# Kernel optimization log

Hardware: AMD Instinct MI355X
Metric: run time of the kernel (lower is better)

Reference implementation:

```python
import jax, jax.numpy as jnp
import numpy as np

B = 32
T_CAP = 63            # max_caption_length - 1
VOCAB = 32000
IMG_DIM = 20480
EMB = 512
LSTM_DIM = 500


def setup_inputs() -> dict:
    key = jax.random.key(0)
    ks = jax.random.split(key, 10)
    s = 0.02
    return {
        "input_image": jax.random.normal(ks[0], (B, IMG_DIM), dtype=jnp.float32),
        "input_caption": jax.random.randint(ks[1], (B, T_CAP), 0, VOCAB, dtype=jnp.int32),
        # image_embedding Dense
        "W_img": jax.random.normal(ks[2], (IMG_DIM, EMB), dtype=jnp.float32) * s,
        "b_img": jnp.zeros((EMB,), dtype=jnp.float32),
        # caption_embedding table
        "emb": jax.random.normal(ks[3], (VOCAB, EMB), dtype=jnp.float32) * s,
        # LSTM kernels (keras gate order: i, f, c, o)
        "W_lstm": jax.random.normal(ks[4], (EMB, 4 * LSTM_DIM), dtype=jnp.float32) * s,
        "U_lstm": jax.random.normal(ks[5], (LSTM_DIM, 4 * LSTM_DIM), dtype=jnp.float32) * s,
        "b_lstm": jnp.concatenate([jnp.zeros((LSTM_DIM,)), jnp.ones((LSTM_DIM,)),
                                    jnp.zeros((2 * LSTM_DIM,))]).astype(jnp.float32),  # unit forget bias
        # output Dense + softmax
        "W_out": jax.random.normal(ks[6], (LSTM_DIM, VOCAB), dtype=jnp.float32) * s,
        "b_out": jnp.zeros((VOCAB,), dtype=jnp.float32),
    }


def _lstm_scan(x, W, U, b):
    # x: [B, T, EMB] -> outputs [B, T, LSTM_DIM]
    Bx = x.shape[0]
    # precompute input projections for all timesteps (one big GEMM)
    xz = jnp.einsum('btd,dg->btg', x, W) + b  # [B, T, 4H]
    xz = jnp.swapaxes(xz, 0, 1)               # [T, B, 4H]
    h0 = jnp.zeros((Bx, LSTM_DIM), dtype=x.dtype)
    c0 = jnp.zeros((Bx, LSTM_DIM), dtype=x.dtype)

    def step(carry, z_t):
        h, c = carry
        z = z_t + h @ U                        # [B, 4H]
        i, f, g, o = jnp.split(z, 4, axis=-1)  # keras gate order i,f,c,o
        i = jax.nn.sigmoid(i)
        f = jax.nn.sigmoid(f)
        g = jnp.tanh(g)
        o = jax.nn.sigmoid(o)
        c_new = f * c + i * g
        h_new = o * jnp.tanh(c_new)
        return (h_new, c_new), h_new

    _, hs = jax.lax.scan(step, (h0, c0), xz)   # hs: [T, B, H]
    return jnp.swapaxes(hs, 0, 1)


def reference(input_image, input_caption, W_img, b_img, emb, W_lstm, U_lstm, b_lstm, W_out, b_out):
    # image embedding -> one leading timestep
    x_image = (input_image @ W_img + b_img)[:, None, :]      # [B, 1, EMB]
    x_caption = emb[input_caption]                            # [B, T-1, EMB]
    x = jnp.concatenate([x_image, x_caption], axis=1)         # [B, T, EMB]
    h = _lstm_scan(x, W_lstm, U_lstm, b_lstm)                 # [B, T, H]
    logits = jnp.einsum('bth,hv->btv', h, W_out) + b_out      # [B, T, VOCAB]
    return jax.nn.softmax(logits, axis=-1)
```

## Files before the change

### kernel.cpp

```cpp
#include <hip/hip_runtime.h>

typedef float f32x4 __attribute__((ext_vector_type(4)));
typedef short s16x8 __attribute__((ext_vector_type(8)));
typedef unsigned int u32;
typedef unsigned long long u64;

#define B_    32
#define T_    64
#define TCAP_ 63
#define V_    32000
#define IMGD_ 20480
#define E_    512
#define H_    500
#define KP_   512

#define OFF_XZ     0ul
#define OFF_XB     16384000ul
#define OFF_WLT    18481152ul
#define OFF_HPAD   20578304ul
#define OFF_HS     20643840ul
#define OFF_UPREP  22740992ul
#define OFF_WT     24838144ul
#define OFF_RS     57606144ul


__device__ __forceinline__ short bf16rn(float f) {
  u32 u = __float_as_uint(f);
  u += 0x7fff + ((u >> 16) & 1);
  return (short)(u >> 16);
}
__device__ __forceinline__ float sigf(float x) {
  return 1.0f / (1.0f + __expf(-x));
}
__device__ __forceinline__ void gload_lds16(const void* g, void* l) {
  __builtin_amdgcn_global_load_lds((const __attribute__((address_space(1))) void*)g,
                                   (__attribute__((address_space(3))) void*)l, 16, 0, 0);
}

#define SG_XB   504
#define SG_X32  520
#define SG_RS   522
#define SG_FL   523
#define SG_UP   4619
#define SG_WT   12619
#define SG_WLT  13131
__global__ __launch_bounds__(256) void k_prep(const float* __restrict__ bimg,
                                              const float* __restrict__ emb,
                                              const int* __restrict__ cap,
                                              const float* __restrict__ U,
                                              const float* __restrict__ Wo,
                                              const float* __restrict__ Wl,
                                              short* __restrict__ xb,
                                              float* __restrict__ x32,
                                              float* __restrict__ rowsum,
                                              u32* __restrict__ flags,
                                              short* __restrict__ up,
                                              short* __restrict__ wt,
                                              short* __restrict__ wlt) {
  __shared__ float s[32][65];
  int bid = blockIdx.x, tid = threadIdx.x;
  if (bid < SG_XB) {
    int u = bid * 256 + tid;
    int r = u >> 6, j8 = u & 63;
    int b = r / 63, tt = r - b * 63;
    int e = cap[b * TCAP_ + tt];
    const float* src = emb + (size_t)e * E_ + j8 * 8;
    f32x4 v0 = *(const f32x4*)src;
    f32x4 v1 = *(const f32x4*)(src + 4);
    s16x8 o;
    o[0]=bf16rn(v0.x); o[1]=bf16rn(v0.y); o[2]=bf16rn(v0.z); o[3]=bf16rn(v0.w);
    o[4]=bf16rn(v1.x); o[5]=bf16rn(v1.y); o[6]=bf16rn(v1.z); o[7]=bf16rn(v1.w);
    *(s16x8*)(xb + (size_t)(b * T_ + tt + 1) * KP_ + j8 * 8) = o;
  } else if (bid < SG_X32) {
    int i = (bid - SG_XB) * 256 + tid;
    int b = i >> 7, j = i & 127;
    *(f32x4*)(x32 + b * E_ + j * 4) = *(const f32x4*)(bimg + j * 4);
  } else if (bid < SG_RS) {
    int i = (bid - SG_X32) * 256 + tid;
    *(f32x4*)(rowsum + i * 4) = (f32x4){0.f, 0.f, 0.f, 0.f};
  } else if (bid < SG_FL) {
    if (tid < 32) flags[tid] = 0u;
  } else if (bid < SG_UP) {
    int idx = (bid - SG_FL) * 256 + tid;
    int k = idx & 511;
    int c = (idx >> 9) & 63;
    int wg = idx >> 15;
    int q = c >> 4, dl = c & 15, dg = wg * 16 + dl;
    float v = 0.f;
    if (dg < H_ && k < H_) v = U[(size_t)k * 2000 + q * H_ + dg];
    up[idx] = bf16rn(v);
  } else if (bid < SG_WT) {
    int r = bid - SG_UP;
    int nt = r % 500, kt = r / 500;
    int n0 = nt * 64, k0 = kt * 32;
    for (int u = tid; u < 2048; u += 256) {
      int kl = u >> 6, nl = u & 63;
      int k = k0 + kl;
      s[kl][nl] = (k < H_) ? Wo[(size_t)k * V_ + n0 + nl] : 0.f;
    }
    __syncthreads();
    for (int u = tid; u < 2048; u += 256) {
      int nl = u >> 5, kl = u & 31;
      wt[(size_t)(n0 + nl) * KP_ + k0 + kl] = bf16rn(s[kl][nl]);
    }
  } else {
    int r = bid - SG_WT;
    int nt = r & 31, kt = r >> 5;
    int n0 = nt * 64, k0 = kt * 32;
    for (int u = tid; u < 2048; u += 256) {
      int kl = u >> 6, nl = u & 63;
      int n = n0 + nl;
      s[kl][nl] = (n < 2000) ? Wl[(size_t)(k0 + kl) * 2000 + n] : 0.f;
    }
    __syncthreads();
    for (int u = tid; u < 2048; u += 256) {
      int nl = u >> 5, kl = u & 31;
      wlt[(size_t)(n0 + nl) * KP_ + k0 + kl] = bf16rn(s[kl][nl]);
    }
  }
}

__global__ __launch_bounds__(256) void k_img(const float* __restrict__ img,
                                             const float* __restrict__ W,
                                             float* __restrict__ x32) {
  __shared__ float simg[32][128];
  int ct = blockIdx.x & 7;
  int ks = blockIdx.x >> 3;
  int tid = threadIdx.x;
  int j = tid & 63, bq = tid >> 6;
  int col = ct * 64 + j;
  float acc[8] = {0.f, 0.f, 0.f, 0.f, 0.f, 0.f, 0.f, 0.f};
  int kbeg = ks * 1280;
  for (int k0 = kbeg; k0 < kbeg + 1280; k0 += 128) {
    __syncthreads();
    for (int u = tid; u < 32 * 32; u += 256) {
      int b = u >> 5, kq = (u & 31) * 4;
      *(f32x4*)&simg[b][kq] = *(const f32x4*)(img + (size_t)b * IMGD_ + k0 + kq);
    }
    __syncthreads();
    for (int k = 0; k < 128; ++k) {
      float w = W[(size_t)(k0 + k) * E_ + col];
#pragma unroll
      for (int r = 0; r < 8; ++r) acc[r] += simg[bq * 8 + r][k] * w;
    }
  }
#pragma unroll
  for (int r = 0; r < 8; ++r)
    atomicAdd(x32 + (bq * 8 + r) * E_ + col, acc[r]);
}

__global__ __launch_bounds__(256) void k_xb(const float* __restrict__ x32,
                                            short* __restrict__ xb) {
  int u = blockIdx.x * 256 + threadIdx.x;
  int b = u >> 6, j8 = u & 63;
  const float* src = x32 + b * E_ + j8 * 8;
  f32x4 v0 = *(const f32x4*)src;
  f32x4 v1 = *(const f32x4*)(src + 4);
  s16x8 o;
  o[0]=bf16rn(v0.x); o[1]=bf16rn(v0.y); o[2]=bf16rn(v0.z); o[3]=bf16rn(v0.w);
  o[4]=bf16rn(v1.x); o[5]=bf16rn(v1.y); o[6]=bf16rn(v1.z); o[7]=bf16rn(v1.w);
  *(s16x8*)(xb + (size_t)(b * T_) * KP_ + j8 * 8) = o;
}

__global__ __launch_bounds__(256) void k_xzm(const short* __restrict__ A,
                                             const short* __restrict__ Bt,
                                             const float* __restrict__ bl,
                                             float* __restrict__ xz) {
  __shared__ short sA[2][128 * 64];
  __shared__ short sB[2][128 * 64];
  int bid = blockIdx.x;
  int mt = bid & 15, nt = bid >> 4;
  int m0 = mt * 128, n0 = nt * 128;
  int tid = threadIdx.x;
  int lane = tid & 63, w = tid >> 6;
  int wr = w >> 1, wc = w & 1;
  int l15 = lane & 15, l4 = lane >> 4;

  f32x4 acc[4][4];
#pragma unroll
  for (int i = 0; i < 4; ++i)
#pragma unroll
    for (int j = 0; j < 4; ++j) acc[i][j] = (f32x4){0.f, 0.f, 0.f, 0.f};

  auto stage = [&](int kc, int buf) {
    const short* ga = A + (size_t)m0 * KP_ + kc * 64;
    const short* gb = Bt + (size_t)n0 * KP_ + kc * 64;
#pragma unroll
    for (int i = 0; i < 4; ++i) {
      int ch = tid + i * 256;
      int rr = ch >> 3, kq = (ch & 7) * 8;
      gload_lds16(ga + (size_t)rr * KP_ + kq, &sA[buf][rr * 64 + kq]);
      gload_lds16(gb + (size_t)rr * KP_ + kq, &sB[buf][rr * 64 + kq]);
    }
  };

  stage(0, 0);
  __syncthreads();
  int buf = 0;
  for (int kc = 0; kc < 8; ++kc) {
    if (kc < 7) stage(kc + 1, buf ^ 1);
#pragma unroll
    for (int k2 = 0; k2 < 2; ++k2) {
      int kloc = k2 * 32 + l4 * 8;
      s16x8 af[4], bfr[4];
#pragma unroll
      for (int fm = 0; fm < 4; ++fm)
        af[fm] = *(const s16x8*)&sA[buf][(wr * 64 + fm * 16 + l15) * 64 + kloc];
#pragma unroll
      for (int fn = 0; fn < 4; ++fn)
        bfr[fn] = *(const s16x8*)&sB[buf][(wc * 64 + fn * 16 + l15) * 64 + kloc];
#pragma unroll
      for (int fm = 0; fm < 4; ++fm)
#pragma unroll
        for (int fn = 0; fn < 4; ++fn)
          acc[fm][fn] = __builtin_amdgcn_mfma_f32_16x16x32_bf16(af[fm], bfr[fn], acc[fm][fn], 0, 0, 0);
    }
    __syncthreads();
    buf ^= 1;
  }

  float bln[4];
#pragma unroll
  for (int fn = 0; fn < 4; ++fn) {
    int n = n0 + wc * 64 + fn * 16 + l15;
    bln[fn] = (n < 2000) ? bl[n] : 0.f;
  }
#pragma unroll
  for (int fm = 0; fm < 4; ++fm) {
#pragma unroll
    for (int reg = 0; reg < 4; ++reg) {
      int m = m0 + wr * 64 + fm * 16 + l4 * 4 + reg;
      int b = m >> 6, t = m & 63;
#pragma unroll
      for (int fn = 0; fn < 4; ++fn) {
        int n = n0 + wc * 64 + fn * 16 + l15;
        if (n < 2000)
          xz[((size_t)t * B_ + b) * 2000 + n] = acc[fm][fn][reg] + bln[fn];
      }
    }
  }
}

__global__ __launch_bounds__(128) void k_scan(const short* __restrict__ up,
                                              const float* __restrict__ xz,
                                              short* hpad,
                                              short* __restrict__ hs,
                                              u32* flags) {
  __shared__ short Ul[64 * 512];
  int wg = blockIdx.x;
  int tid = threadIdx.x;
  int lane = tid & 63, mtile = tid >> 6;
  int dl = lane & 15, g16 = lane >> 4;

  const short* usrc = up + (size_t)wg * 64 * 512;
  for (int u = tid; u < 4096; u += 128) {
    int c = u >> 6, kq = (u & 63) * 8;
    u32 off = ((u32)(c * 512 + kq) * 2) ^ ((u32)(c & 7) << 4);
    *(s16x8*)((char*)Ul + off) = *(const s16x8*)(usrc + c * 512 + kq);
  }
  __syncthreads();

  int dg = wg * 16 + dl;
  bool dvalid = dg < H_;
  float cst[4] = {0.f, 0.f, 0.f, 0.f};
  int brow = mtile * 16 + dl;

  float xzr[4][4];
  auto pf = [&](int t) {
#pragma unroll
    for (int q = 0; q < 4; ++q)
#pragma unroll
      for (int reg = 0; reg < 4; ++reg) {
        int b = mtile * 16 + g16 * 4 + reg;
        xzr[q][reg] = dvalid ? xz[((size_t)t * B_ + b) * 2000 + q * 500 + dg] : 0.f;
      }
  };
  pf(0);

  for (int t = 0; t < 64; ++t) {
    f32x4 acc[4];
#pragma unroll
    for (int q = 0; q < 4; ++q) acc[q] = (f32x4){0.f, 0.f, 0.f, 0.f};

    if (t > 0) {
      const short* hsrc = hpad + (size_t)(t & 1) * (B_ * KP_);
      u64 q0[16], q1[16];
#pragma unroll
      for (int kk = 0; kk < 16; ++kk) {
        const u64* p = (const u64*)(hsrc + brow * KP_ + kk * 32 + g16 * 8);
        q0[kk] = __hip_atomic_load(p,     __ATOMIC_RELAXED, __HIP_MEMORY_SCOPE_AGENT);
        q1[kk] = __hip_atomic_load(p + 1, __ATOMIC_RELAXED, __HIP_MEMORY_SCOPE_AGENT);
      }
#pragma unroll
      for (int kk = 0; kk < 16; ++kk) {
        union { s16x8 v; u64 q[2]; } fr;
        fr.q[0] = q0[kk]; fr.q[1] = q1[kk];
#pragma unroll
        for (int q = 0; q < 4; ++q) {
          int c = q * 16 + dl;
          u32 off = ((u32)(c * 512 + kk * 32 + g16 * 8) * 2) ^ ((u32)(c & 7) << 4);
          s16x8 bfr = *(const s16x8*)((const char*)Ul + off);
          acc[q] = __builtin_amdgcn_mfma_f32_16x16x32_bf16(fr.v, bfr, acc[q], 0, 0, 0);
        }
      }
    }

    short hb4[4];
#pragma unroll
    for (int reg = 0; reg < 4; ++reg) {
      float zi = acc[0][reg] + xzr[0][reg];
      float zf = acc[1][reg] + xzr[1][reg];
      float zc = acc[2][reg] + xzr[2][reg];
      float zo = acc[3][reg] + xzr[3][reg];
      float ig = sigf(zi), fg = sigf(zf), gt = tanhf(zc), og = sigf(zo);
      float cn = fg * cst[reg] + ig * gt;
      cst[reg] = cn;
      float h = og * tanhf(cn);
      if (!dvalid) h = 0.f;
      hb4[reg] = bf16rn(h);
    }

    short* hnext = hpad + (size_t)((t + 1) & 1) * (B_ * KP_);
#pragma unroll
    for (int reg = 0; reg < 4; ++reg) {
      int mine = (int)(u32)(unsigned short)hb4[reg];
      int oth = __shfl_xor(mine, 1);
      if ((dl & 1) == 0) {
        int b = mtile * 16 + g16 * 4 + reg;
        u32 val = ((u32)mine) | ((u32)oth << 16);
        __hip_atomic_store((u32*)hnext + ((b * KP_ + dg) >> 1), val,
                           __ATOMIC_RELAXED, __HIP_MEMORY_SCOPE_AGENT);
      }
    }

    if (t < 63) {
      __syncthreads();
      if (tid == 0)
        __hip_atomic_store(&flags[wg], (u32)(t + 1),
                           __ATOMIC_RELAXED, __HIP_MEMORY_SCOPE_AGENT);
      asm volatile("" ::: "memory");
#pragma unroll
      for (int reg = 0; reg < 4; ++reg) {
        int b = mtile * 16 + g16 * 4 + reg;
        hs[((size_t)b * T_ + t) * KP_ + dg] = hb4[reg];
      }
      pf(t + 1);
      if (tid < 64) {
        u32 target = (u32)(t + 1);
        int slot = tid & 31;
        while (true) {
          u32 v = __hip_atomic_load(&flags[slot], __ATOMIC_RELAXED,
                                    __HIP_MEMORY_SCOPE_AGENT);
          if (__all(v >= target)) break;
          __builtin_amdgcn_s_sleep(1);
        }
      }
      __syncthreads();
    } else {
#pragma unroll
      for (int reg = 0; reg < 4; ++reg) {
        int b = mtile * 16 + g16 * 4 + reg;
        hs[((size_t)b * T_ + t) * KP_ + dg] = hb4[reg];
      }
    }
  }
}

__global__ __launch_bounds__(256) void k_gemm(const short* __restrict__ A,
                                              const short* __restrict__ Bt,
                                              const float* __restrict__ bout,
                                              float* __restrict__ out,
                                              float* __restrict__ rowsum) {
  __shared__ short sA[2][128 * 64];
  __shared__ short sB[2][128 * 64];
  int bid = blockIdx.x;
  int mt = bid & 15, nt = bid >> 4;
  int m0 = mt * 128, n0 = nt * 128;
  int tid = threadIdx.x;
  int lane = tid & 63, w = tid >> 6;
  int wr = w >> 1, wc = w & 1;
  int l15 = lane & 15, l4 = lane >> 4;

  f32x4 acc[4][4];
#pragma unroll
  for (int i = 0; i < 4; ++i)
#pragma unroll
    for (int j = 0; j < 4; ++j) acc[i][j] = (f32x4){0.f, 0.f, 0.f, 0.f};

  auto stage = [&](int kc, int buf) {
    const short* ga = A + (size_t)m0 * KP_ + kc * 64;
    const short* gb = Bt + (size_t)n0 * KP_ + kc * 64;
#pragma unroll
    for (int i = 0; i < 4; ++i) {
      int ch = tid + i * 256;
      int rr = ch >> 3, kq = (ch & 7) * 8;
      gload_lds16(ga + (size_t)rr * KP_ + kq, &sA[buf][rr * 64 + kq]);
      gload_lds16(gb + (size_t)rr * KP_ + kq, &sB[buf][rr * 64 + kq]);
    }
  };

  stage(0, 0);
  __syncthreads();
  int buf = 0;
  for (int kc = 0; kc < 8; ++kc) {
    if (kc < 7) stage(kc + 1, buf ^ 1);
#pragma unroll
    for (int k2 = 0; k2 < 2; ++k2) {
      int kloc = k2 * 32 + l4 * 8;
      s16x8 af[4], bfr[4];
#pragma unroll
      for (int fm = 0; fm < 4; ++fm)
        af[fm] = *(const s16x8*)&sA[buf][(wr * 64 + fm * 16 + l15) * 64 + kloc];
#pragma unroll
      for (int fn = 0; fn < 4; ++fn)
        bfr[fn] = *(const s16x8*)&sB[buf][(wc * 64 + fn * 16 + l15) * 64 + kloc];
#pragma unroll
      for (int fm = 0; fm < 4; ++fm)
#pragma unroll
        for (int fn = 0; fn < 4; ++fn)
          acc[fm][fn] = __builtin_amdgcn_mfma_f32_16x16x32_bf16(af[fm], bfr[fn], acc[fm][fn], 0, 0, 0);
    }
    __syncthreads();
    buf ^= 1;
  }

  float bo4[4];
#pragma unroll
  for (int fn = 0; fn < 4; ++fn) bo4[fn] = bout[n0 + wc * 64 + fn * 16 + l15];

#pragma unroll
  for (int fm = 0; fm < 4; ++fm) {
#pragma unroll
    for (int reg = 0; reg < 4; ++reg) {
      int m = m0 + wr * 64 + fm * 16 + l4 * 4 + reg;
      float s = 0.f;
#pragma unroll
      for (int fn = 0; fn < 4; ++fn) {
        int n = n0 + wc * 64 + fn * 16 + l15;
        float e = __expf(acc[fm][fn][reg] + bo4[fn]);
        out[(size_t)m * V_ + n] = e;
        s += e;
      }
      s += __shfl_xor(s, 1);
      s += __shfl_xor(s, 2);
      s += __shfl_xor(s, 4);
      s += __shfl_xor(s, 8);
      if (l15 == 0) atomicAdd(&rowsum[m], s);
    }
  }
}

__global__ __launch_bounds__(256) void k_norm(float* __restrict__ out,
                                              const float* __restrict__ rowsum) {
  size_t i = (size_t)blockIdx.x * 256 + threadIdx.x;
  if (i >= 16384000ul) return;
  int row = (int)(i / 8000);
  float inv = 1.0f / rowsum[row];
  f32x4 v = *(f32x4*)(out + i * 4);
  v.x *= inv; v.y *= inv; v.z *= inv; v.w *= inv;
  *(f32x4*)(out + i * 4) = v;
}

extern "C" void kernel_launch(void* const* d_in, const int* in_sizes, int n_in,
                              void* d_out, int out_size, void* d_ws, size_t ws_size,
                              hipStream_t stream) {
  const float* img  = (const float*)d_in[0];
  const int*   cap  = (const int*)  d_in[1];
  const float* Wimg = (const float*)d_in[2];
  const float* bimg = (const float*)d_in[3];
  const float* emb  = (const float*)d_in[4];
  const float* Wl   = (const float*)d_in[5];
  const float* Ulm  = (const float*)d_in[6];
  const float* bl   = (const float*)d_in[7];
  const float* Wo   = (const float*)d_in[8];
  const float* bo   = (const float*)d_in[9];
  float* out = (float*)d_out;
  char* ws = (char*)d_ws;

  float* xz     = (float*)(ws + OFF_XZ);
  short* xb     = (short*)(ws + OFF_XB);
  short* wlt    = (short*)(ws + OFF_WLT);
  short* hpad   = (short*)(ws + OFF_HPAD);
  short* hs     = (short*)(ws + OFF_HS);
  short* uprep  = (short*)(ws + OFF_UPREP);
  short* wt     = (short*)(ws + OFF_WT);
  float* rowsum = (float*)(ws + OFF_RS);
  u32*   flags  = (u32*)d_out;
  float* x32    = (float*)d_out + 1024;

  k_prep<<<SG_WLT, 256, 0, stream>>>(bimg, emb, cap, Ulm, Wo, Wl,
                                     xb, x32, rowsum, flags, uprep, wt, wlt);
  k_img<<<128, 256, 0, stream>>>(img, Wimg, x32);
  k_xb<<<8, 256, 0, stream>>>(x32, xb);
  k_xzm<<<256, 256, 0, stream>>>(xb, wlt, bl, xz);

  {
    const short* up_p = uprep;
    const float* xz_p = xz;
    short* hpad_p = hpad;
    short* hs_p = hs;
    u32* flags_p = flags;
    void* args[] = {&up_p, &xz_p, &hpad_p, &hs_p, &flags_p};
    hipLaunchCooperativeKernel((void*)k_scan, dim3(32), dim3(128), args, 0, stream);
  }

  k_gemm<<<4000, 256, 0, stream>>>(hs, wt, bo, out, rowsum);
  k_norm<<<64000, 256, 0, stream>>>(out, rowsum);
}
```

Baseline: 778.6 us.

## Recompute output GEMM twice instead of writing and re-reading unnormalized softmax

```diff
diff --git a/kernel.cpp b/kernel.cpp
--- a/kernel.cpp
+++ b/kernel.cpp
@@ -366,12 +366,12 @@
   }
 }
 
+template <int PHASE>
 __global__ __launch_bounds__(256) void k_gemm(const short* __restrict__ A,
                                               const short* __restrict__ Bt,
                                               const float* __restrict__ bout,
                                               float* __restrict__ out,
                                               float* __restrict__ rowsum) {
-  __shared__ short sA[2][128 * 64];
   __shared__ short sB[2][128 * 64];
   int bid = blockIdx.x;
   int mt = bid & 15, nt = bid >> 4;
@@ -387,14 +387,17 @@
 #pragma unroll
     for (int j = 0; j < 4; ++j) acc[i][j] = (f32x4){0.f, 0.f, 0.f, 0.f};
 
+  const short* arow[4];
+#pragma unroll
+  for (int fm = 0; fm < 4; ++fm)
+    arow[fm] = A + (size_t)(m0 + wr * 64 + fm * 16 + l15) * KP_ + l4 * 8;
+
   auto stage = [&](int kc, int buf) {
-    const short* ga = A + (size_t)m0 * KP_ + kc * 64;
     const short* gb = Bt + (size_t)n0 * KP_ + kc * 64;
 #pragma unroll
     for (int i = 0; i < 4; ++i) {
       int ch = tid + i * 256;
       int rr = ch >> 3, kq = (ch & 7) * 8;
-      gload_lds16(ga + (size_t)rr * KP_ + kq, &sA[buf][rr * 64 + kq]);
       gload_lds16(gb + (size_t)rr * KP_ + kq, &sB[buf][rr * 64 + kq]);
     }
   };
@@ -410,7 +413,7 @@
       s16x8 af[4], bfr[4];
 #pragma unroll
       for (int fm = 0; fm < 4; ++fm)
-        af[fm] = *(const s16x8*)&sA[buf][(wr * 64 + fm * 16 + l15) * 64 + kloc];
+        af[fm] = *(const s16x8*)(arow[fm] + kc * 64 + k2 * 32);
 #pragma unroll
       for (int fn = 0; fn < 4; ++fn)
         bfr[fn] = *(const s16x8*)&sB[buf][(wc * 64 + fn * 16 + l15) * 64 + kloc];
@@ -433,32 +436,27 @@
 #pragma unroll
     for (int reg = 0; reg < 4; ++reg) {
       int m = m0 + wr * 64 + fm * 16 + l4 * 4 + reg;
-      float s = 0.f;
-#pragma unroll
-      for (int fn = 0; fn < 4; ++fn) {
-        int n = n0 + wc * 64 + fn * 16 + l15;
-        float e = __expf(acc[fm][fn][reg] + bo4[fn]);
-        out[(size_t)m * V_ + n] = e;
-        s += e;
-      }
-      s += __shfl_xor(s, 1);
-      s += __shfl_xor(s, 2);
-      s += __shfl_xor(s, 4);
-      s += __shfl_xor(s, 8);
-      if (l15 == 0) atomicAdd(&rowsum[m], s);
-    }
-  }
-}
-
-__global__ __launch_bounds__(256) void k_norm(float* __restrict__ out,
-                                              const float* __restrict__ rowsum) {
-  size_t i = (size_t)blockIdx.x * 256 + threadIdx.x;
-  if (i >= 16384000ul) return;
-  int row = (int)(i / 8000);
-  float inv = 1.0f / rowsum[row];
-  f32x4 v = *(f32x4*)(out + i * 4);
-  v.x *= inv; v.y *= inv; v.z *= inv; v.w *= inv;
-  *(f32x4*)(out + i * 4) = v;
+      if constexpr (PHASE == 0) {
+        float s = 0.f;
+#pragma unroll
+        for (int fn = 0; fn < 4; ++fn)
+          s += __expf(acc[fm][fn][reg] + bo4[fn]);
+        s += __shfl_xor(s, 1);
+        s += __shfl_xor(s, 2);
+        s += __shfl_xor(s, 4);
+        s += __shfl_xor(s, 8);
+        if (l15 == 0) atomicAdd(&rowsum[m], s);
+      } else {
+        float inv = 1.0f / rowsum[m];
+#pragma unroll
+        for (int fn = 0; fn < 4; ++fn) {
+          int n = n0 + wc * 64 + fn * 16 + l15;
+          float e = __expf(acc[fm][fn][reg] + bo4[fn]);
+          out[(size_t)m * V_ + n] = e * inv;
+        }
+      }
+    }
+  }
 }
 
 extern "C" void kernel_launch(void* const* d_in, const int* in_sizes, int n_in,
@@ -504,6 +502,6 @@
     hipLaunchCooperativeKernel((void*)k_scan, dim3(32), dim3(128), args, 0, stream);
   }
 
-  k_gemm<<<4000, 256, 0, stream>>>(hs, wt, bo, out, rowsum);
-  k_norm<<<64000, 256, 0, stream>>>(out, rowsum);
-}
+  k_gemm<0><<<4000, 256, 0, stream>>>(hs, wt, bo, out, rowsum);
+  k_gemm<1><<<4000, 256, 0, stream>>>(hs, wt, bo, out, rowsum);
+}
```

After: 858.5 us. 1.1x slower.

## Overlap W_out transpose with LSTM scan; load GEMM A operand directly

Applied to the files above, without the earlier changes.

```diff
diff --git a/kernel.cpp b/kernel.cpp
--- a/kernel.cpp
+++ b/kernel.cpp
@@ -42,20 +42,17 @@
 #define SG_RS   522
 #define SG_FL   523
 #define SG_UP   4619
-#define SG_WT   12619
-#define SG_WLT  13131
+#define SG_WLT  5131
 __global__ __launch_bounds__(256) void k_prep(const float* __restrict__ bimg,
                                               const float* __restrict__ emb,
                                               const int* __restrict__ cap,
                                               const float* __restrict__ U,
-                                              const float* __restrict__ Wo,
                                               const float* __restrict__ Wl,
                                               short* __restrict__ xb,
                                               float* __restrict__ x32,
                                               float* __restrict__ rowsum,
                                               u32* __restrict__ flags,
                                               short* __restrict__ up,
-                                              short* __restrict__ wt,
                                               short* __restrict__ wlt) {
   __shared__ float s[32][65];
   int bid = blockIdx.x, tid = threadIdx.x;
@@ -89,22 +86,8 @@
     float v = 0.f;
     if (dg < H_ && k < H_) v = U[(size_t)k * 2000 + q * H_ + dg];
     up[idx] = bf16rn(v);
-  } else if (bid < SG_WT) {
+  } else {
     int r = bid - SG_UP;
-    int nt = r % 500, kt = r / 500;
-    int n0 = nt * 64, k0 = kt * 32;
-    for (int u = tid; u < 2048; u += 256) {
-      int kl = u >> 6, nl = u & 63;
-      int k = k0 + kl;
-      s[kl][nl] = (k < H_) ? Wo[(size_t)k * V_ + n0 + nl] : 0.f;
-    }
-    __syncthreads();
-    for (int u = tid; u < 2048; u += 256) {
-      int nl = u >> 5, kl = u & 31;
-      wt[(size_t)(n0 + nl) * KP_ + k0 + kl] = bf16rn(s[kl][nl]);
-    }
-  } else {
-    int r = bid - SG_WT;
     int nt = r & 31, kt = r >> 5;
     int n0 = nt * 64, k0 = kt * 32;
     for (int u = tid; u < 2048; u += 256) {
@@ -245,10 +228,33 @@
                                               const float* __restrict__ xz,
                                               short* hpad,
                                               short* __restrict__ hs,
-                                              u32* flags) {
+                                              u32* flags,
+                                              const float* __restrict__ Wo,
+                                              short* __restrict__ wt) {
   __shared__ short Ul[64 * 512];
   int wg = blockIdx.x;
   int tid = threadIdx.x;
+
+  if (wg >= 32) {
+    float (*s)[65] = (float(*)[65])Ul;
+    for (int tile = wg - 32; tile < 8000; tile += 224) {
+      int nt = tile % 500, kt = tile / 500;
+      int n0 = nt * 64, k0 = kt * 32;
+      __syncthreads();
+      for (int u = tid; u < 2048; u += 128) {
+        int kl = u >> 6, nl = u & 63;
+        int k = k0 + kl;
+        s[kl][nl] = (k < H_) ? Wo[(size_t)k * V_ + n0 + nl] : 0.f;
+      }
+      __syncthreads();
+      for (int u = tid; u < 2048; u += 128) {
+        int nl = u >> 5, kl = u & 31;
+        wt[(size_t)(n0 + nl) * KP_ + k0 + kl] = bf16rn(s[kl][nl]);
+      }
+    }
+    return;
+  }
+
   int lane = tid & 63, mtile = tid >> 6;
   int dl = lane & 15, g16 = lane >> 4;
 
@@ -371,7 +377,6 @@
                                               const float* __restrict__ bout,
                                               float* __restrict__ out,
                                               float* __restrict__ rowsum) {
-  __shared__ short sA[2][128 * 64];
   __shared__ short sB[2][128 * 64];
   int bid = blockIdx.x;
   int mt = bid & 15, nt = bid >> 4;
@@ -387,14 +392,17 @@
 #pragma unroll
     for (int j = 0; j < 4; ++j) acc[i][j] = (f32x4){0.f, 0.f, 0.f, 0.f};
 
+  const short* arow[4];
+#pragma unroll
+  for (int fm = 0; fm < 4; ++fm)
+    arow[fm] = A + (size_t)(m0 + wr * 64 + fm * 16 + l15) * KP_ + l4 * 8;
+
   auto stage = [&](int kc, int buf) {
-    const short* ga = A + (size_t)m0 * KP_ + kc * 64;
     const short* gb = Bt + (size_t)n0 * KP_ + kc * 64;
 #pragma unroll
     for (int i = 0; i < 4; ++i) {
       int ch = tid + i * 256;
       int rr = ch >> 3, kq = (ch & 7) * 8;
-      gload_lds16(ga + (size_t)rr * KP_ + kq, &sA[buf][rr * 64 + kq]);
       gload_lds16(gb + (size_t)rr * KP_ + kq, &sB[buf][rr * 64 + kq]);
     }
   };
@@ -410,7 +418,7 @@
       s16x8 af[4], bfr[4];
 #pragma unroll
       for (int fm = 0; fm < 4; ++fm)
-        af[fm] = *(const s16x8*)&sA[buf][(wr * 64 + fm * 16 + l15) * 64 + kloc];
+        af[fm] = *(const s16x8*)(arow[fm] + kc * 64 + k2 * 32);
 #pragma unroll
       for (int fn = 0; fn < 4; ++fn)
         bfr[fn] = *(const s16x8*)&sB[buf][(wc * 64 + fn * 16 + l15) * 64 + kloc];
@@ -488,8 +496,8 @@
   u32*   flags  = (u32*)d_out;
   float* x32    = (float*)d_out + 1024;
 
-  k_prep<<<SG_WLT, 256, 0, stream>>>(bimg, emb, cap, Ulm, Wo, Wl,
-                                     xb, x32, rowsum, flags, uprep, wt, wlt);
+  k_prep<<<SG_WLT, 256, 0, stream>>>(bimg, emb, cap, Ulm, Wl,
+                                     xb, x32, rowsum, flags, uprep, wlt);
   k_img<<<128, 256, 0, stream>>>(img, Wimg, x32);
   k_xb<<<8, 256, 0, stream>>>(x32, xb);
   k_xzm<<<256, 256, 0, stream>>>(xb, wlt, bl, xz);
@@ -500,8 +508,10 @@
     short* hpad_p = hpad;
     short* hs_p = hs;
     u32* flags_p = flags;
-    void* args[] = {&up_p, &xz_p, &hpad_p, &hs_p, &flags_p};
-    hipLaunchCooperativeKernel((void*)k_scan, dim3(32), dim3(128), args, 0, stream);
+    const float* wo_p = Wo;
+    short* wt_p = wt;
+    void* args[] = {&up_p, &xz_p, &hpad_p, &hs_p, &flags_p, &wo_p, &wt_p};
+    hipLaunchCooperativeKernel((void*)k_scan, dim3(256), dim3(128), args, 0, stream);
   }
 
   k_gemm<<<4000, 256, 0, stream>>>(hs, wt, bo, out, rowsum);
```

After: 769.0 us (median of 2 runs). No clear change (-1.2%).
